# Performance work log

Measured on AMD Instinct MI355X. Metric: run time of the kernel, lower is better.

The kernel has to match this reference:

```python
import jax, jax.numpy as jnp
import numpy as np

DIM_V = 512
H = 8
EPS = 1e-5

def _layernorm(x, g, b):
    mu = jnp.mean(x, axis=-1, keepdims=True)
    var = jnp.var(x, axis=-1, keepdims=True)
    return (x - mu) * jax.lax.rsqrt(var + EPS) * g + b

def setup_inputs() -> dict:
    key = jax.random.key(0)
    ks = jax.random.split(key, 10)
    B, Nq, Nk, dq, dk, dv = 8, 1024, 1024, 512, 512, DIM_V
    def lin(k, fan_in, shape):
        bound = 1.0 / np.sqrt(fan_in)
        return jax.random.uniform(k, shape, jnp.float32, -bound, bound)
    return {
        "Q": jax.random.normal(ks[0], (B, Nq, dq), jnp.float32),
        "K": jax.random.normal(ks[1], (B, Nk, dk), jnp.float32),
        "Wq": lin(ks[2], dq, (dv, dq)), "bq": lin(ks[3], dq, (dv,)),
        "Wk": lin(ks[4], dk, (dv, dk)), "bk": lin(ks[5], dk, (dv,)),
        "Wv": lin(ks[6], dk, (dv, dk)), "bv": lin(ks[7], dk, (dv,)),
        "Wo": lin(ks[8], dv, (dv, dv)), "bo": lin(ks[9], dv, (dv,)),
        "g0": jnp.ones((dv,), jnp.float32), "beta0": jnp.zeros((dv,), jnp.float32),
        "g1": jnp.ones((dv,), jnp.float32), "beta1": jnp.zeros((dv,), jnp.float32),
    }

def reference(Q, K, Wq, bq, Wk, bk, Wv, bv, Wo, bo, g0, beta0, g1, beta1):
    B, Nq, _ = Q.shape
    Nk = K.shape[1]
    d_h = DIM_V // H
    Qp = Q @ Wq.T + bq            # [B,Nq,dv]
    Kp = K @ Wk.T + bk            # [B,Nk,dv]
    Vp = K @ Wv.T + bv            # [B,Nk,dv]
    # split heads along feature dim (matches torch split(dim_split,2)+cat(0))
    Qh = Qp.reshape(B, Nq, H, d_h).transpose(0, 2, 1, 3)  # [B,H,Nq,dh]
    Kh = Kp.reshape(B, Nk, H, d_h).transpose(0, 2, 1, 3)
    Vh = Vp.reshape(B, Nk, H, d_h).transpose(0, 2, 1, 3)
    # NOTE: original scales by sqrt(dim_V), the FULL model dim
    scores = jnp.einsum('bhnd,bhmd->bhnm', Qh, Kh) / jnp.sqrt(jnp.float32(DIM_V))
    A = jax.nn.softmax(scores, axis=-1)                   # [B,H,Nq,Nk]
    Oh = Qh + jnp.einsum('bhnm,bhmd->bhnd', A, Vh)        # residual on projected Q
    O = Oh.transpose(0, 2, 1, 3).reshape(B, Nq, DIM_V)
    O = _layernorm(O, g0, beta0)
    O = O + jax.nn.relu(O @ Wo.T + bo)
    O = _layernorm(O, g1, beta1)
    return O
```

## Files before the change

kernel.cpp:

```cpp
#include <hip/hip_runtime.h>
#include <hip/hip_bf16.h>

typedef __hip_bfloat16 bf16;
typedef short bf16x8 __attribute__((ext_vector_type(8)));
typedef float f32x4 __attribute__((ext_vector_type(4)));
typedef unsigned int u32;

static __device__ __forceinline__ float bfu2f(unsigned short u) { return __uint_as_float((u32)u << 16); }
static __device__ __forceinline__ u32 pack2(float a, float b) {
    return (u32)__bfloat16_as_ushort(__float2bfloat16(a))
         | ((u32)__bfloat16_as_ushort(__float2bfloat16(b)) << 16);
}
static __device__ __forceinline__ float wave_sum(float v) {
    #pragma unroll
    for (int off = 32; off > 0; off >>= 1) v += __shfl_xor(v, off);
    return v;
}

static __device__ __forceinline__ void gll16(const bf16* g, bf16* l) {
    __builtin_amdgcn_global_load_lds((const __attribute__((address_space(1))) void*)g,
                                     (__attribute__((address_space(3))) void*)l,
                                     16, 0, 0);
}

__global__ __launch_bounds__(256) void castall(const float* __restrict__ Q,  const float* __restrict__ K,
                                               const float* __restrict__ Wq, const float* __restrict__ Wk,
                                               const float* __restrict__ Wv, const float* __restrict__ Wo,
                                               bf16* __restrict__ dQ,  bf16* __restrict__ dK,
                                               bf16* __restrict__ dWq, bf16* __restrict__ dWk,
                                               bf16* __restrict__ dWv, bf16* __restrict__ dWo)
{
    const int b = blockIdx.x;
    const float* src; bf16* dst; size_t off;
    if (b < 1024)      { src = Q;  dst = dQ;  off = (size_t)b * 4096; }
    else if (b < 2048) { src = K;  dst = dK;  off = (size_t)(b - 1024) * 4096; }
    else {
        const int wb = b - 2048, wi = wb >> 6;
        off = (size_t)(wb & 63) * 4096;
        src = wi == 0 ? Wq : wi == 1 ? Wk : wi == 2 ? Wv : Wo;
        dst = wi == 0 ? dWq : wi == 1 ? dWk : wi == 2 ? dWv : dWo;
    }
    const size_t p = off + threadIdx.x * 16;
    const float4 v0 = *(const float4*)(src + p);
    const float4 v1 = *(const float4*)(src + p + 4);
    const float4 v2 = *(const float4*)(src + p + 8);
    const float4 v3 = *(const float4*)(src + p + 12);
    uint4 o0, o1;
    o0.x = pack2(v0.x, v0.y); o0.y = pack2(v0.z, v0.w);
    o0.z = pack2(v1.x, v1.y); o0.w = pack2(v1.z, v1.w);
    o1.x = pack2(v2.x, v2.y); o1.y = pack2(v2.z, v2.w);
    o1.z = pack2(v3.x, v3.y); o1.w = pack2(v3.z, v3.w);
    *(uint4*)(dst + p)     = o0;
    *(uint4*)(dst + p + 8) = o1;
}

__global__ __launch_bounds__(256) void gemm_qkv(const bf16* __restrict__ Aq, const bf16* __restrict__ Ak,
                                                const bf16* __restrict__ Wq, const bf16* __restrict__ Wk,
                                                const bf16* __restrict__ Wv,
                                                const float* __restrict__ bq, const float* __restrict__ bk,
                                                const float* __restrict__ bv,
                                                bf16* __restrict__ oQ, bf16* __restrict__ oK,
                                                bf16* __restrict__ oV)
{
    __shared__ bf16 Xs[128 * 64];
    __shared__ bf16 Ws[128 * 64];

    const int tid = threadIdx.x, lane = tid & 63, wave = tid >> 6;
    const int yy = blockIdx.y, wi = yy >> 2;
    const bf16* A     = wi == 0 ? Aq : Ak;
    const bf16* W     = wi == 0 ? Wq : wi == 1 ? Wk : Wv;
    const float* bias = wi == 0 ? bq : wi == 1 ? bk : bv;
    bf16* out         = wi == 0 ? oQ : wi == 1 ? oK : oV;
    const bool vmode  = (wi == 2);
    const int bm = blockIdx.x * 128;
    const int bn = (yy & 3) * 128;

    const int srow = tid >> 3;
    const int sg8  = (((tid & 7) ^ (srow & 7)) * 8);
    const int wm = (wave >> 1) * 64, wn = (wave & 1) * 64;
    const int fr = lane & 15, fq = lane >> 4;

    f32x4 acc[4][4] = {};
    const bf16* Ap = A + (size_t)(bm + srow) * 512 + sg8;
    const bf16* Wp = W + (size_t)(bn + srow) * 512 + sg8;
    const int ld = 8 * tid;

    for (int k0 = 0; k0 < 512; k0 += 64) {
        __syncthreads();
        #pragma unroll
        for (int c = 0; c < 4; c++) {
            gll16(Ap + k0 + (size_t)(32 * c) * 512, Xs + ld + 2048 * c);
            gll16(Wp + k0 + (size_t)(32 * c) * 512, Ws + ld + 2048 * c);
        }
        __syncthreads();

        #pragma unroll
        for (int c2 = 0; c2 < 2; c2++) {
            bf16x8 fx[4], fw[4];
            #pragma unroll
            for (int i = 0; i < 4; i++) {
                const int rx = wm + 16 * i + fr;
                const int rw = wn + 16 * i + fr;
                fx[i] = *(const bf16x8*)(&Xs[rx * 64 + (((c2 * 4 + fq) ^ (rx & 7)) * 8)]);
                fw[i] = *(const bf16x8*)(&Ws[rw * 64 + (((c2 * 4 + fq) ^ (rw & 7)) * 8)]);
            }
            if (vmode) {
                #pragma unroll
                for (int i = 0; i < 4; i++)
                    #pragma unroll
                    for (int j = 0; j < 4; j++)
                        acc[i][j] = __builtin_amdgcn_mfma_f32_16x16x32_bf16(fx[i], fw[j], acc[i][j], 0, 0, 0);
            } else {
                #pragma unroll
                for (int i = 0; i < 4; i++)
                    #pragma unroll
                    for (int j = 0; j < 4; j++)
                        acc[i][j] = __builtin_amdgcn_mfma_f32_16x16x32_bf16(fw[i], fx[j], acc[i][j], 0, 0, 0);
            }
        }
    }

    if (!vmode) {
        #pragma unroll
        for (int i = 0; i < 4; i++) {
            const int colb = bn + wn + 16 * i + 4 * fq;
            const float4 b4 = *(const float4*)(bias + colb);
            const int h = colb >> 6, d0 = colb & 63;
            #pragma unroll
            for (int j = 0; j < 4; j++) {
                const int n = bm + wm + 16 * j + fr;
                const int b = n >> 10, nn = n & 1023;
                uint2 pk;
                pk.x = pack2(acc[i][j][0] + b4.x, acc[i][j][1] + b4.y);
                pk.y = pack2(acc[i][j][2] + b4.z, acc[i][j][3] + b4.w);
                *(uint2*)(out + ((size_t)(b * 8 + h) * 1024 + nn) * 64 + d0) = pk;
            }
        }
    } else {
        #pragma unroll
        for (int i = 0; i < 4; i++) {
            const int n0 = bm + wm + 16 * i + 4 * fq;
            const int b = n0 >> 10, nn = n0 & 1023;
            #pragma unroll
            for (int j = 0; j < 4; j++) {
                const int col = bn + wn + 16 * j + fr;
                const float bv2 = bias[col];
                const int h = col >> 6, d = col & 63;
                uint2 pk;
                pk.x = pack2(acc[i][j][0] + bv2, acc[i][j][1] + bv2);
                pk.y = pack2(acc[i][j][2] + bv2, acc[i][j][3] + bv2);
                *(uint2*)(out + ((size_t)(b * 8 + h) * 64 + d) * 1024 + nn) = pk;
            }
        }
    }
}

__global__ __launch_bounds__(256) void gemm_o(const bf16* __restrict__ A,
                                              const bf16* __restrict__ W,
                                              const float* __restrict__ bias,
                                              bf16* __restrict__ out)
{
    __shared__ bf16 Xs[64 * 64];
    __shared__ bf16 Ws[128 * 64];

    const int tid = threadIdx.x, lane = tid & 63, wave = tid >> 6;
    const int bm = blockIdx.x * 64;
    const int bn = blockIdx.y * 128;

    const int srow = tid >> 3;
    const int sg8  = (((tid & 7) ^ (srow & 7)) * 8);
    const int wn = wave * 32;
    const int fr = lane & 15, fq = lane >> 4;

    f32x4 acc[2][4] = {};
    const bf16* Ap = A + (size_t)(bm + srow) * 512 + sg8;
    const bf16* Wp = W + (size_t)(bn + srow) * 512 + sg8;
    const int ld = 8 * tid;

    for (int k0 = 0; k0 < 512; k0 += 64) {
        __syncthreads();
        #pragma unroll
        for (int c = 0; c < 2; c++)
            gll16(Ap + k0 + (size_t)(32 * c) * 512, Xs + ld + 2048 * c);
        #pragma unroll
        for (int c = 0; c < 4; c++)
            gll16(Wp + k0 + (size_t)(32 * c) * 512, Ws + ld + 2048 * c);
        __syncthreads();

        #pragma unroll
        for (int c2 = 0; c2 < 2; c2++) {
            bf16x8 fx[4], fw[2];
            #pragma unroll
            for (int j = 0; j < 4; j++) {
                const int rx = 16 * j + fr;
                fx[j] = *(const bf16x8*)(&Xs[rx * 64 + (((c2 * 4 + fq) ^ (rx & 7)) * 8)]);
            }
            #pragma unroll
            for (int i = 0; i < 2; i++) {
                const int rw = wn + 16 * i + fr;
                fw[i] = *(const bf16x8*)(&Ws[rw * 64 + (((c2 * 4 + fq) ^ (rw & 7)) * 8)]);
            }
            #pragma unroll
            for (int i = 0; i < 2; i++)
                #pragma unroll
                for (int j = 0; j < 4; j++)
                    acc[i][j] = __builtin_amdgcn_mfma_f32_16x16x32_bf16(fw[i], fx[j], acc[i][j], 0, 0, 0);
        }
    }

    #pragma unroll
    for (int i = 0; i < 2; i++) {
        const int colb = bn + wn + 16 * i + 4 * fq;
        const float4 b4 = *(const float4*)(bias + colb);
        #pragma unroll
        for (int j = 0; j < 4; j++) {
            const int row = bm + 16 * j + fr;
            uint2 pk;
            pk.x = pack2(acc[i][j][0] + b4.x, acc[i][j][1] + b4.y);
            pk.y = pack2(acc[i][j][2] + b4.z, acc[i][j][3] + b4.w);
            *(uint2*)(out + (size_t)row * 512 + colb) = pk;
        }
    }
}

__global__ __launch_bounds__(256) void attn_mfma(const bf16* __restrict__ Qh,
                                                 const bf16* __restrict__ Kh,
                                                 const bf16* __restrict__ VhT,
                                                 bf16* __restrict__ Oc)
{
    __shared__ bf16 Ks[64 * 64];
    __shared__ bf16 Vs[64 * 64];
    __shared__ bf16 Ps[4][2][16 * 72];

    const int tid = threadIdx.x, lane = tid & 63, w = tid >> 6;
    const int id = blockIdx.x;
    const int bh = (id & 7) * 8 + (id >> 6);
    const int wq = ((id >> 3) & 7) * 128 + w * 32;

    const bf16* Qb = Qh  + ((size_t)bh * 1024 + wq) * 64;
    const bf16* Kb = Kh  + (size_t)bh * 1024 * 64;
    const bf16* Vb = VhT + (size_t)bh * 64 * 1024;

    const int fl = lane & 15, fq = lane >> 4;
    const int flk = fl & 7;
    const int gA = (fq ^ flk) * 8;
    const int gB = ((4 | fq) ^ flk) * 8;

    bf16x8 qf[2][2];
    #pragma unroll
    for (int t = 0; t < 2; t++) {
        qf[t][0] = *(const bf16x8*)(Qb + (16 * t + fl) * 64 + fq * 8);
        qf[t][1] = *(const bf16x8*)(Qb + (16 * t + fl) * 64 + 32 + fq * 8);
    }

    f32x4 o[2][4] = {};
    float lsum[2] = {0.f, 0.f};
    const float sc2 = 0.04419417382415922f * 1.4426950408889634f;

    const int srow = tid >> 3;
    const int sg8  = (((tid & 7) ^ (srow & 7)) * 8);
    const bf16* KbR  = Kb + (size_t)srow * 64 + sg8;
    const bf16* VbR0 = Vb + (size_t)srow * 1024 + sg8;
    const bf16* VbR1 = Vb + (size_t)(srow + 32) * 1024 + sg8;
    const int ld = 8 * tid;

    for (int kt = 0; kt < 16; kt++) {
        const int m0 = kt * 64;
        __syncthreads();
        gll16(KbR + (size_t)m0 * 64,        Ks + ld);
        gll16(KbR + (size_t)(m0 + 32) * 64, Ks + 2048 + ld);
        gll16(VbR0 + m0,                    Vs + ld);
        gll16(VbR1 + m0,                    Vs + 2048 + ld);
        __syncthreads();

        bf16x8 kf[4][2];
        #pragma unroll
        for (int tm = 0; tm < 4; tm++) {
            kf[tm][0] = *(const bf16x8*)(&Ks[(16 * tm + fl) * 64 + gA]);
            kf[tm][1] = *(const bf16x8*)(&Ks[(16 * tm + fl) * 64 + gB]);
        }

        #pragma unroll
        for (int t = 0; t < 2; t++) {
            f32x4 st[4] = {};
            #pragma unroll
            for (int tm = 0; tm < 4; tm++) {
                st[tm] = __builtin_amdgcn_mfma_f32_16x16x32_bf16(kf[tm][0], qf[t][0], st[tm], 0, 0, 0);
                st[tm] = __builtin_amdgcn_mfma_f32_16x16x32_bf16(kf[tm][1], qf[t][1], st[tm], 0, 0, 0);
            }
            #pragma unroll
            for (int tm = 0; tm < 4; tm++) {
                float p0 = __builtin_amdgcn_exp2f(st[tm][0] * sc2);
                float p1 = __builtin_amdgcn_exp2f(st[tm][1] * sc2);
                float p2 = __builtin_amdgcn_exp2f(st[tm][2] * sc2);
                float p3 = __builtin_amdgcn_exp2f(st[tm][3] * sc2);
                lsum[t] += (p0 + p1) + (p2 + p3);
                uint2 pk;
                pk.x = pack2(p0, p1);
                pk.y = pack2(p2, p3);
                *(uint2*)(&Ps[w][t][fl * 72 + 16 * tm + fq * 4]) = pk;
            }
        }

        bf16x8 vf[4][2];
        #pragma unroll
        for (int jd = 0; jd < 4; jd++) {
            vf[jd][0] = *(const bf16x8*)(&Vs[(16 * jd + fl) * 64 + gA]);
            vf[jd][1] = *(const bf16x8*)(&Vs[(16 * jd + fl) * 64 + gB]);
        }
        #pragma unroll
        for (int t = 0; t < 2; t++) {
            bf16x8 pf0 = *(const bf16x8*)(&Ps[w][t][fl * 72 + fq * 8]);
            bf16x8 pf1 = *(const bf16x8*)(&Ps[w][t][fl * 72 + 32 + fq * 8]);
            #pragma unroll
            for (int jd = 0; jd < 4; jd++) {
                o[t][jd] = __builtin_amdgcn_mfma_f32_16x16x32_bf16(vf[jd][0], pf0, o[t][jd], 0, 0, 0);
                o[t][jd] = __builtin_amdgcn_mfma_f32_16x16x32_bf16(vf[jd][1], pf1, o[t][jd], 0, 0, 0);
            }
        }
    }

    const int b = bh >> 3, h = bh & 7;
    #pragma unroll
    for (int t = 0; t < 2; t++) {
        float ls = lsum[t];
        ls += __shfl_xor(ls, 16);
        ls += __shfl_xor(ls, 32);
        const float linv = 1.f / ls;
        const size_t obase = ((size_t)(b * 1024 + wq + 16 * t + fl)) * 512 + h * 64;
        #pragma unroll
        for (int jd = 0; jd < 4; jd++) {
            const ushort4 qr = *(const ushort4*)(Qb + (16 * t + fl) * 64 + 16 * jd + fq * 4);
            uint2 w2;
            w2.x = pack2(o[t][jd][0] * linv + bfu2f(qr.x), o[t][jd][1] * linv + bfu2f(qr.y));
            w2.y = pack2(o[t][jd][2] * linv + bfu2f(qr.z), o[t][jd][3] * linv + bfu2f(qr.w));
            *(uint2*)(&Oc[obase + 16 * jd + fq * 4]) = w2;
        }
    }
}

__global__ __launch_bounds__(256) void ln0(const bf16* __restrict__ X,
                                           const float* __restrict__ g,
                                           const float* __restrict__ be,
                                           bf16* __restrict__ Y)
{
    const int lane = threadIdx.x & 63;
    const int row = blockIdx.x * 4 + (threadIdx.x >> 6);
    const size_t base = (size_t)row * 512 + lane * 8;
    const bf16x8 xv = *(const bf16x8*)(X + base);
    float x[8];
    #pragma unroll
    for (int j = 0; j < 8; j++) x[j] = bfu2f((unsigned short)xv[j]);
    float s = 0.f, s2 = 0.f;
    #pragma unroll
    for (int j = 0; j < 8; j++) { s += x[j]; s2 += x[j] * x[j]; }
    s = wave_sum(s); s2 = wave_sum(s2);
    const float mean = s * (1.f / 512.f);
    const float var = s2 * (1.f / 512.f) - mean * mean;
    const float rs = rsqrtf(fmaxf(var, 0.f) + 1e-5f);
    const float4 gv0 = *(const float4*)(g + lane * 8);
    const float4 gv1 = *(const float4*)(g + lane * 8 + 4);
    const float4 bv0 = *(const float4*)(be + lane * 8);
    const float4 bv1 = *(const float4*)(be + lane * 8 + 4);
    uint4 ov;
    ov.x = pack2((x[0]-mean)*rs*gv0.x + bv0.x, (x[1]-mean)*rs*gv0.y + bv0.y);
    ov.y = pack2((x[2]-mean)*rs*gv0.z + bv0.z, (x[3]-mean)*rs*gv0.w + bv0.w);
    ov.z = pack2((x[4]-mean)*rs*gv1.x + bv1.x, (x[5]-mean)*rs*gv1.y + bv1.y);
    ov.w = pack2((x[6]-mean)*rs*gv1.z + bv1.z, (x[7]-mean)*rs*gv1.w + bv1.w);
    *(uint4*)(Y + base) = ov;
}

__global__ __launch_bounds__(256) void ln1(const bf16* __restrict__ X,
                                           const bf16* __restrict__ R,
                                           const float* __restrict__ g,
                                           const float* __restrict__ be,
                                           float* __restrict__ Y)
{
    const int lane = threadIdx.x & 63;
    const int row = blockIdx.x * 4 + (threadIdx.x >> 6);
    const size_t base = (size_t)row * 512 + lane * 8;
    const bf16x8 xv = *(const bf16x8*)(X + base);
    const bf16x8 rv = *(const bf16x8*)(R + base);
    float x[8];
    #pragma unroll
    for (int j = 0; j < 8; j++)
        x[j] = bfu2f((unsigned short)rv[j]) + fmaxf(bfu2f((unsigned short)xv[j]), 0.f);
    float s = 0.f, s2 = 0.f;
    #pragma unroll
    for (int j = 0; j < 8; j++) { s += x[j]; s2 += x[j] * x[j]; }
    s = wave_sum(s); s2 = wave_sum(s2);
    const float mean = s * (1.f / 512.f);
    const float var = s2 * (1.f / 512.f) - mean * mean;
    const float rs = rsqrtf(fmaxf(var, 0.f) + 1e-5f);
    const float4 gv0 = *(const float4*)(g + lane * 8);
    const float4 gv1 = *(const float4*)(g + lane * 8 + 4);
    const float4 bv0 = *(const float4*)(be + lane * 8);
    const float4 bv1 = *(const float4*)(be + lane * 8 + 4);
    float4 y0, y1;
    y0.x = (x[0]-mean)*rs*gv0.x + bv0.x; y0.y = (x[1]-mean)*rs*gv0.y + bv0.y;
    y0.z = (x[2]-mean)*rs*gv0.z + bv0.z; y0.w = (x[3]-mean)*rs*gv0.w + bv0.w;
    y1.x = (x[4]-mean)*rs*gv1.x + bv1.x; y1.y = (x[5]-mean)*rs*gv1.y + bv1.y;
    y1.z = (x[6]-mean)*rs*gv1.z + bv1.z; y1.w = (x[7]-mean)*rs*gv1.w + bv1.w;
    *(float4*)(Y + base)     = y0;
    *(float4*)(Y + base + 4) = y1;
}

extern "C" void kernel_launch(void* const* d_in, const int* in_sizes, int n_in,
                              void* d_out, int out_size, void* d_ws, size_t ws_size,
                              hipStream_t stream)
{
    const float* Q   = (const float*)d_in[0];
    const float* K   = (const float*)d_in[1];
    const float* Wq  = (const float*)d_in[2];
    const float* bq  = (const float*)d_in[3];
    const float* Wk  = (const float*)d_in[4];
    const float* bk  = (const float*)d_in[5];
    const float* Wv  = (const float*)d_in[6];
    const float* bv  = (const float*)d_in[7];
    const float* Wo  = (const float*)d_in[8];
    const float* bo  = (const float*)d_in[9];
    const float* g0  = (const float*)d_in[10];
    const float* be0 = (const float*)d_in[11];
    const float* g1  = (const float*)d_in[12];
    const float* be1 = (const float*)d_in[13];
    float* out = (float*)d_out;

    const size_t NQK = (size_t)8 * 1024 * 512;
    const size_t NW  = (size_t)512 * 512;
    bf16* ws   = (bf16*)d_ws;
    bf16* cQ   = ws;
    bf16* cK   = cQ + NQK;
    bf16* cWq  = cK + NQK;
    bf16* cWk  = cWq + NW;
    bf16* cWv  = cWk + NW;
    bf16* cWo  = cWv + NW;
    bf16* pQh  = cWo + NW;
    bf16* pKh  = pQh + NQK;
    bf16* pVhT = pKh + NQK;
    bf16* pOc  = (bf16*)d_out;
    bf16* pO1  = pKh;
    bf16* pTmp = pQh;

    castall<<<2304, 256, 0, stream>>>(Q, K, Wq, Wk, Wv, Wo, cQ, cK, cWq, cWk, cWv, cWo);
    gemm_qkv<<<dim3(64, 12), 256, 0, stream>>>(cQ, cK, cWq, cWk, cWv, bq, bk, bv, pQh, pKh, pVhT);
    attn_mfma<<<512, 256, 0, stream>>>(pQh, pKh, pVhT, pOc);
    ln0<<<2048, 256, 0, stream>>>(pOc, g0, be0, pO1);
    gemm_o<<<dim3(128, 4), 256, 0, stream>>>(pO1, cWo, bo, pTmp);
    ln1<<<2048, 256, 0, stream>>>(pTmp, pO1, g1, be1, out);
}
```

Measured before the change: 186.0 us.

## Double-buffer K tiles in LDS and load V fragments directly from global

The attention kernel now double-buffers the K tile in shared memory and prefetches the next tile with async global-to-LDS loads, using manual vmcnt waits and raw barriers instead of two __syncthreads per iteration. V fragments are read straight from global memory into registers, with no staging through LDS. s_setprio brackets are added around the MFMA blocks. This aims to overlap K loads with compute and cut LDS traffic and barrier stalls. The cost is uncoalesced direct global V reads and fragile hand-counted waitcnt values.

```diff
diff --git a/kernel.cpp b/kernel.cpp
--- a/kernel.cpp
+++ b/kernel.cpp
@@ -228,8 +228,7 @@
                                                  const bf16* __restrict__ VhT,
                                                  bf16* __restrict__ Oc)
 {
-    __shared__ bf16 Ks[64 * 64];
-    __shared__ bf16 Vs[64 * 64];
+    __shared__ bf16 Ks[2][64 * 64];
     __shared__ bf16 Ps[4][2][16 * 72];
 
     const int tid = threadIdx.x, lane = tid & 63, w = tid >> 6;
@@ -259,35 +258,54 @@
 
     const int srow = tid >> 3;
     const int sg8  = (((tid & 7) ^ (srow & 7)) * 8);
-    const bf16* KbR  = Kb + (size_t)srow * 64 + sg8;
-    const bf16* VbR0 = Vb + (size_t)srow * 1024 + sg8;
-    const bf16* VbR1 = Vb + (size_t)(srow + 32) * 1024 + sg8;
+    const bf16* KbR = Kb + (size_t)srow * 64 + sg8;
     const int ld = 8 * tid;
 
+    const bf16* VbL = Vb + (size_t)fl * 1024 + fq * 8;
+
+    gll16(KbR,           &Ks[0][0] + ld);
+    gll16(KbR + 32 * 64, &Ks[0][0] + 2048 + ld);
+
+    #pragma unroll 1
     for (int kt = 0; kt < 16; kt++) {
         const int m0 = kt * 64;
-        __syncthreads();
-        gll16(KbR + (size_t)m0 * 64,        Ks + ld);
-        gll16(KbR + (size_t)(m0 + 32) * 64, Ks + 2048 + ld);
-        gll16(VbR0 + m0,                    Vs + ld);
-        gll16(VbR1 + m0,                    Vs + 2048 + ld);
-        __syncthreads();
+        const bf16* Ksc = &Ks[kt & 1][0];
+
+        bf16x8 vf[4][2];
+        #pragma unroll
+        for (int jd = 0; jd < 4; jd++) {
+            const bf16* vp = VbL + (size_t)(16 * jd) * 1024 + m0;
+            vf[jd][0] = *(const bf16x8*)(vp);
+            vf[jd][1] = *(const bf16x8*)(vp + 32);
+        }
+
+        if (kt < 15) {
+            bf16* Kn = &Ks[(kt + 1) & 1][0];
+            gll16(KbR + (size_t)(m0 + 64) * 64, Kn + ld);
+            gll16(KbR + (size_t)(m0 + 96) * 64, Kn + 2048 + ld);
+            asm volatile("s_waitcnt vmcnt(10)" ::: "memory");
+        } else {
+            asm volatile("s_waitcnt vmcnt(8)" ::: "memory");
+        }
+        __builtin_amdgcn_s_barrier();
 
         bf16x8 kf[4][2];
         #pragma unroll
         for (int tm = 0; tm < 4; tm++) {
-            kf[tm][0] = *(const bf16x8*)(&Ks[(16 * tm + fl) * 64 + gA]);
-            kf[tm][1] = *(const bf16x8*)(&Ks[(16 * tm + fl) * 64 + gB]);
+            kf[tm][0] = *(const bf16x8*)(&Ksc[(16 * tm + fl) * 64 + gA]);
+            kf[tm][1] = *(const bf16x8*)(&Ksc[(16 * tm + fl) * 64 + gB]);
         }
 
         #pragma unroll
         for (int t = 0; t < 2; t++) {
             f32x4 st[4] = {};
+            __builtin_amdgcn_s_setprio(1);
             #pragma unroll
             for (int tm = 0; tm < 4; tm++) {
                 st[tm] = __builtin_amdgcn_mfma_f32_16x16x32_bf16(kf[tm][0], qf[t][0], st[tm], 0, 0, 0);
                 st[tm] = __builtin_amdgcn_mfma_f32_16x16x32_bf16(kf[tm][1], qf[t][1], st[tm], 0, 0, 0);
             }
+            __builtin_amdgcn_s_setprio(0);
             #pragma unroll
             for (int tm = 0; tm < 4; tm++) {
                 float p0 = __builtin_amdgcn_exp2f(st[tm][0] * sc2);
@@ -302,22 +320,19 @@
             }
         }
 
-        bf16x8 vf[4][2];
-        #pragma unroll
-        for (int jd = 0; jd < 4; jd++) {
-            vf[jd][0] = *(const bf16x8*)(&Vs[(16 * jd + fl) * 64 + gA]);
-            vf[jd][1] = *(const bf16x8*)(&Vs[(16 * jd + fl) * 64 + gB]);
-        }
         #pragma unroll
         for (int t = 0; t < 2; t++) {
             bf16x8 pf0 = *(const bf16x8*)(&Ps[w][t][fl * 72 + fq * 8]);
             bf16x8 pf1 = *(const bf16x8*)(&Ps[w][t][fl * 72 + 32 + fq * 8]);
+            __builtin_amdgcn_s_setprio(1);
             #pragma unroll
             for (int jd = 0; jd < 4; jd++) {
                 o[t][jd] = __builtin_amdgcn_mfma_f32_16x16x32_bf16(vf[jd][0], pf0, o[t][jd], 0, 0, 0);
                 o[t][jd] = __builtin_amdgcn_mfma_f32_16x16x32_bf16(vf[jd][1], pf1, o[t][jd], 0, 0, 0);
             }
-        }
+            __builtin_amdgcn_s_setprio(0);
+        }
+        __builtin_amdgcn_s_barrier();
     }
 
     const int b = bh >> 3, h = bh & 7;
```

Result: slower. 195.3 us (+5.0%).
